# Performance work log

Hardware: AMD Instinct MI355X
Metric: run time of the kernel (lower is better)

## Reference

```python
import jax, jax.numpy as jnp
import numpy as np

N_NODES = 100000
N_EDGES = 3200000
N_GRAPHS = 512
HID = 64
OUT = 10


def setup_inputs() -> dict:
    key = jax.random.key(0)
    ks = jax.random.split(key, 10)
    x = jax.random.normal(ks[0], (N_NODES,), dtype=jnp.float32)
    edge_index = jax.random.randint(ks[1], (2, N_EDGES), 0, N_NODES, dtype=jnp.int64)
    batch = jnp.sort(jax.random.randint(ks[2], (N_NODES,), 0, N_GRAPHS, dtype=jnp.int64))
    # GCNConv weights (glorot) and zero biases, Linear layer params
    W1 = jax.random.normal(ks[3], (1, HID), dtype=jnp.float32) * (1.0 / np.sqrt(1 + HID))
    b1 = jnp.zeros((HID,), dtype=jnp.float32)
    W2 = jax.random.normal(ks[4], (HID, HID), dtype=jnp.float32) * (1.0 / np.sqrt(2 * HID))
    b2 = jnp.zeros((HID,), dtype=jnp.float32)
    Wl = jax.random.normal(ks[5], (2 * HID, OUT), dtype=jnp.float32) * (1.0 / np.sqrt(2 * HID))
    bl = jnp.zeros((OUT,), dtype=jnp.float32)
    return {"x": x, "edge_index": edge_index, "batch": batch,
            "W1": W1, "b1": b1, "W2": W2, "b2": b2, "Wl": Wl, "bl": bl}


def reference(x, edge_index, batch, W1, b1, W2, b2, Wl, bl):
    N = x.shape[0]
    loop = jnp.arange(N, dtype=edge_index.dtype)
    src = jnp.concatenate([edge_index[0], loop])  # add self-loops
    dst = jnp.concatenate([edge_index[1], loop])
    # symmetric GCN normalization: D^{-1/2} A_hat D^{-1/2}
    deg = jax.ops.segment_sum(jnp.ones_like(dst, dtype=jnp.float32), dst, num_segments=N)
    dinv = jax.lax.rsqrt(jnp.maximum(deg, 1.0))
    norm = (dinv[src] * dinv[dst])[:, None]  # [E+N, 1]

    def gcn(h, W, b):
        m = (h @ W)[src] * norm  # transform then gather messages
        return jax.ops.segment_sum(m, dst, num_segments=N) + b

    h0 = x[:, None]  # [N, 1] (dropout is identity at eval)
    x1 = jax.nn.relu(gcn(h0, W1, b1))
    x2 = jax.nn.relu(gcn(x1, W2, b2))
    xj = jnp.concatenate([x1, x2], axis=-1)  # JK 'cat' -> [N, 128]
    # global mean pool per graph
    cnt = jax.ops.segment_sum(jnp.ones((N,), jnp.float32), batch, num_segments=N_GRAPHS)
    pooled = jax.ops.segment_sum(xj, batch, num_segments=N_GRAPHS) / jnp.maximum(cnt, 1.0)[:, None]
    return pooled @ Wl + bl  # [G, 10]
```

## Files before the change

kernel.cpp:

```cpp
#include <hip/hip_runtime.h>
#include <hip/hip_bf16.h>

#define N_NODES 100000
#define N_EDGES 3200000
#define N_GRAPHS 512
#define HID 64
#define OUT_DIM 10

#define NPB 64
#define NB  1563
#define CAP 2432
#define CAP2 (CAP + NPB)


__global__ __launch_bounds__(256) void k_part(const int4* __restrict__ src4,
                                              const int4* __restrict__ dst4,
                                              unsigned* __restrict__ bcur,
                                              unsigned* __restrict__ ebuf) {
    __shared__ unsigned hist[NB];
    int tid = threadIdx.x;
    for (int i = tid; i < NB; i += 256) hist[i] = 0;
    __syncthreads();
    int base4 = (blockIdx.x * 256 + tid) * 2;
    int4 s0 = make_int4(-1, -1, -1, -1), s1 = s0;
    int4 d0 = make_int4(0, 0, 0, 0), d1 = d0;
    if (base4 < N_EDGES / 4)     { s0 = src4[base4];     d0 = dst4[base4]; }
    if (base4 + 1 < N_EDGES / 4) { s1 = src4[base4 + 1]; d1 = dst4[base4 + 1]; }
    int sv[8] = { s0.x, s0.y, s0.z, s0.w, s1.x, s1.y, s1.z, s1.w };
    int dv[8] = { d0.x, d0.y, d0.z, d0.w, d1.x, d1.y, d1.z, d1.w };
    int bk[8]; unsigned rk[8];
    #pragma unroll
    for (int k = 0; k < 8; k++) {
        bk[k] = dv[k] >> 6;
        rk[k] = (sv[k] >= 0) ? atomicAdd(&hist[bk[k]], 1u) : 0u;
    }
    __syncthreads();
    for (int i = tid; i < NB; i += 256) {
        unsigned c = hist[i];
        hist[i] = c ? atomicAdd(&bcur[i], c) : 0u;
    }
    __syncthreads();
    #pragma unroll
    for (int k = 0; k < 8; k++) {
        if (sv[k] >= 0) {
            unsigned dl = (unsigned)(dv[k] & 63);
            ebuf[(size_t)bk[k] * CAP + hist[bk[k]] + rk[k]] = (dl << 17) | (unsigned)sv[k];
        }
    }
}

__global__ __launch_bounds__(256) void k_buck1(unsigned* __restrict__ ebuf,
                                               const unsigned* __restrict__ bcur,
                                               const float* __restrict__ x,
                                               unsigned* __restrict__ deg,
                                               float* __restrict__ dinv,
                                               float* __restrict__ g1) {
    __shared__ unsigned cnt[NPB];
    int b = blockIdx.x, tid = threadIdx.x;
    if (tid < NPB) cnt[tid] = 0;
    __syncthreads();
    int ec = (int)bcur[b];
    unsigned* eb = ebuf + (size_t)b * CAP;
    for (int i = tid; i < ec; i += 256) {
        unsigned w = eb[i];
        unsigned rk = atomicAdd(&cnt[(w >> 17) & 63], 1u);
        eb[i] = w | (rk << 23);
    }
    __syncthreads();
    int n0 = b * NPB;
    int nn = min(NPB, N_NODES - n0);
    if (tid < nn) {
        unsigned c = cnt[tid];
        float dn = 1.0f / sqrtf((float)c + 1.0f);
        deg[n0 + tid] = c;
        dinv[n0 + tid] = dn;
        g1[n0 + tid] = dn * x[n0 + tid];
    }
}

__global__ __launch_bounds__(256) void k_buck2(const unsigned* __restrict__ ebuf,
                                               const unsigned* __restrict__ bcur,
                                               const float* __restrict__ g1,
                                               const float* __restrict__ dinv,
                                               const float* __restrict__ x,
                                               float2* __restrict__ sd) {
    __shared__ float sacc[NPB];
    int b = blockIdx.x, tid = threadIdx.x;
    if (tid < NPB) sacc[tid] = 0.f;
    __syncthreads();
    int ec = (int)bcur[b];
    const unsigned* eb = ebuf + (size_t)b * CAP;
    for (int i = tid; i < ec; i += 256) {
        unsigned w = eb[i];
        atomicAdd(&sacc[(w >> 17) & 63], g1[w & 0x1FFFFu]);
    }
    __syncthreads();
    int n0 = b * NPB;
    int nn = min(NPB, N_NODES - n0);
    if (tid < nn) {
        float dn = dinv[n0 + tid];
        float s = dn * (sacc[tid] + dn * x[n0 + tid]);
        sd[n0 + tid] = make_float2(s, dn);
    }
}

__global__ __launch_bounds__(256) void k_buck3(const unsigned* __restrict__ ebuf,
                                               const unsigned* __restrict__ bcur,
                                               const unsigned* __restrict__ deg,
                                               const float2* __restrict__ sd,
                                               const int* __restrict__ batch,
                                               const float* __restrict__ W1,
                                               const float* __restrict__ b1,
                                               const float* __restrict__ W2,
                                               const float* __restrict__ b2,
                                               float* __restrict__ pooled) {
    __shared__ __align__(16) float2 stage2[CAP2];
    __shared__ float w2ls[HID * HID];
    __shared__ int offs[NPB + 1];
    __shared__ int degs[NPB];
    int b = blockIdx.x, tid = threadIdx.x;
    int lane = tid & 63, wv = tid >> 6;
    int n0 = b * NPB;
    int nn = min(NPB, N_NODES - n0);
    for (int i = tid; i < HID * HID; i += 256) w2ls[i] = W2[i];
    if (wv == 0) {
        int d = (lane < nn) ? (int)deg[n0 + lane] : 0;
        degs[lane] = d;
        int dp = (d + 1) & ~1;
        int sum = dp;
        #pragma unroll
        for (int o = 1; o < 64; o <<= 1) {
            int t = __shfl_up(sum, o, 64);
            if (lane >= o) sum += t;
        }
        offs[lane + 1] = sum;
        offs[lane]     = sum - dp;
        if (lane == 0) offs[0] = 0;
    }
    float w1 = W1[lane], bb1 = b1[lane], bb2 = b2[lane];
    __syncthreads();
    int ec = (int)bcur[b];
    const unsigned* eb = ebuf + (size_t)b * CAP;
    for (int i = tid; i < ec; i += 256) {
        unsigned w = eb[i];
        stage2[offs[(w >> 17) & 63] + (w >> 23)] = sd[w & 0x1FFFFu];
    }
    __syncthreads();
    const float4* stv = (const float4*)stage2;
    int curg = -1;
    float pacc1 = 0.f, pacc2 = 0.f;
    for (int n = wv; n < nn; n += 4) {
        int lo = offs[n];
        int m = degs[n];
        float acca = 0.f, accb = 0.f;
        int half = m >> 1;
        int p0 = lo >> 1;
        for (int k = 0; k < half; k++) {
            float4 e = stv[p0 + k];
            acca = fmaf(e.y, fmaxf(fmaf(e.x, w1, bb1), 0.f), acca);
            accb = fmaf(e.w, fmaxf(fmaf(e.z, w1, bb1), 0.f), accb);
        }
        if (m & 1) {
            float2 e0 = stage2[lo + m - 1];
            acca = fmaf(e0.y, fmaxf(fmaf(e0.x, w1, bb1), 0.f), acca);
        }
        float2 self = sd[n0 + n];
        float t = fmaxf(fmaf(self.x, w1, bb1), 0.f);
        float a = self.y * (acca + accb + self.y * t);
        float acc2a = bb2, acc2b = 0.f;
        #pragma unroll
        for (int j = 0; j < HID; j += 2) {
            float aj0 = __int_as_float(__builtin_amdgcn_readlane(__float_as_int(a), j));
            float aj1 = __int_as_float(__builtin_amdgcn_readlane(__float_as_int(a), j + 1));
            acc2a = fmaf(aj0, w2ls[j * HID + lane], acc2a);
            acc2b = fmaf(aj1, w2ls[(j + 1) * HID + lane], acc2b);
        }
        float x2v = fmaxf(acc2a + acc2b, 0.f);
        int g = batch[n0 + n];
        if (g != curg) {
            if (curg >= 0) {
                atomicAdd(&pooled[curg * 2 * HID + lane], pacc1);
                atomicAdd(&pooled[curg * 2 * HID + HID + lane], pacc2);
            }
            curg = g; pacc1 = 0.f; pacc2 = 0.f;
        }
        pacc1 += t;
        pacc2 += x2v;
    }
    if (curg >= 0) {
        atomicAdd(&pooled[curg * 2 * HID + lane], pacc1);
        atomicAdd(&pooled[curg * 2 * HID + HID + lane], pacc2);
    }
}

__global__ __launch_bounds__(128) void k_head(const float* __restrict__ pooled,
                                              const int* __restrict__ batch,
                                              const float* __restrict__ Wl,
                                              const float* __restrict__ bl,
                                              float* __restrict__ out) {
    int g = blockIdx.x;
    int t = threadIdx.x;
    int lo1 = 0, hi1 = N_NODES;
    while (lo1 < hi1) { int mid = (lo1 + hi1) >> 1; if (batch[mid] < g) lo1 = mid + 1; else hi1 = mid; }
    int lo2 = lo1, hi2 = N_NODES;
    while (lo2 < hi2) { int mid = (lo2 + hi2) >> 1; if (batch[mid] < g + 1) lo2 = mid + 1; else hi2 = mid; }
    float denom = fmaxf((float)(lo2 - lo1), 1.f);
    __shared__ float pl[2 * HID];
    pl[t] = pooled[g * 2 * HID + t] / denom;
    __syncthreads();
    if (t < OUT_DIM) {
        float r = bl[t];
        #pragma unroll 16
        for (int j = 0; j < 2 * HID; j++) r = fmaf(pl[j], Wl[j * OUT_DIM + t], r);
        out[g * OUT_DIM + t] = r;
    }
}

extern "C" void kernel_launch(void* const* d_in, const int* in_sizes, int n_in,
                              void* d_out, int out_size, void* d_ws, size_t ws_size,
                              hipStream_t stream) {
    const float* x      = (const float*)d_in[0];
    const int*   ei     = (const int*)d_in[1];
    const int*   batch  = (const int*)d_in[2];
    const float* W1     = (const float*)d_in[3];
    const float* b1     = (const float*)d_in[4];
    const float* W2     = (const float*)d_in[5];
    const float* b2     = (const float*)d_in[6];
    const float* Wl     = (const float*)d_in[7];
    const float* bl     = (const float*)d_in[8];
    float* out = (float*)d_out;

    const int* src = ei;
    const int* dst = ei + N_EDGES;

    char* p = (char*)d_ws;
    auto alloc = [&](size_t bytes) { void* r = (void*)p; p += (bytes + 255) & ~(size_t)255; return r; };
    unsigned* bcur   = (unsigned*)alloc(NB * 4);
    unsigned* ebuf   = (unsigned*)alloc((size_t)NB * CAP * 4);
    unsigned* deg    = (unsigned*)alloc(N_NODES * 4);
    float*    dinv   = (float*)alloc(N_NODES * 4);
    float*    g1     = (float*)alloc(N_NODES * 4);
    float2*   sd     = (float2*)alloc((size_t)N_NODES * 8);
    float*    pooled = (float*)alloc((size_t)N_GRAPHS * 2 * HID * 4);

    hipMemsetAsync(bcur, 0, NB * 4, stream);
    hipMemsetAsync(pooled, 0, (size_t)N_GRAPHS * 2 * HID * 4, stream);

    const int TB = 256;
    int pbl = (N_EDGES / 8 + TB - 1) / TB;

    k_part <<<pbl, TB, 0, stream>>>((const int4*)src, (const int4*)dst, bcur, ebuf);
    k_buck1<<<NB, TB, 0, stream>>>(ebuf, bcur, x, deg, dinv, g1);
    k_buck2<<<NB, TB, 0, stream>>>(ebuf, bcur, g1, dinv, x, sd);
    k_buck3<<<NB, TB, 0, stream>>>(ebuf, bcur, deg, sd, batch, W1, b1, W2, b2, pooled);
    k_head <<<N_GRAPHS, 128, 0, stream>>>(pooled, batch, Wl, bl, out);
}
```

Before: 266.9 us.

## Replace single-pass edge bucketing with two-level coarse/fine counting sort

Edges are now first scattered into 391 coarse buckets of 256 destination nodes, using larger per-block edge chunks and fewer histogram bins. A second kernel then counting-sorts each coarse bucket by local destination in shared memory and writes a dst-sorted buffer plus per-64-node fine ranges. The later kernels read contiguous fine ranges, which removes the per-edge rank rewrite and gives more coalesced scatter writes in the partition step. The cost is an extra full pass over the edge buffer, a second edge buffer, and a serial single-thread prefix scan over 256 bins per coarse block.

Measured after the change: 251.5 us. -5.8%, faster.

```diff
diff --git a/kernel.cpp b/kernel.cpp
--- a/kernel.cpp
+++ b/kernel.cpp
@@ -7,68 +7,91 @@
 #define HID 64
 #define OUT_DIM 10
 
+#define NPC 256
+#define NCB 391
+#define CAPA 8960
 #define NPB 64
-#define NB  1563
-#define CAP 2432
-#define CAP2 (CAP + NPB)
-
-
-__global__ __launch_bounds__(256) void k_part(const int4* __restrict__ src4,
-                                              const int4* __restrict__ dst4,
-                                              unsigned* __restrict__ bcur,
-                                              unsigned* __restrict__ ebuf) {
-    __shared__ unsigned hist[NB];
+#define NFB 1563
+#define CAPF 2432
+#define CAP2 (CAPF + NPB)
+
+
+__global__ __launch_bounds__(256) void k_partA(const int4* __restrict__ src4,
+                                               const int4* __restrict__ dst4,
+                                               unsigned* __restrict__ bcurA,
+                                               unsigned* __restrict__ ebufA) {
+    __shared__ unsigned hist[NCB];
+    __shared__ unsigned short rk16[4096];
     int tid = threadIdx.x;
-    for (int i = tid; i < NB; i += 256) hist[i] = 0;
-    __syncthreads();
-    int base4 = (blockIdx.x * 256 + tid) * 2;
-    int4 s0 = make_int4(-1, -1, -1, -1), s1 = s0;
-    int4 d0 = make_int4(0, 0, 0, 0), d1 = d0;
-    if (base4 < N_EDGES / 4)     { s0 = src4[base4];     d0 = dst4[base4]; }
-    if (base4 + 1 < N_EDGES / 4) { s1 = src4[base4 + 1]; d1 = dst4[base4 + 1]; }
-    int sv[8] = { s0.x, s0.y, s0.z, s0.w, s1.x, s1.y, s1.z, s1.w };
-    int dv[8] = { d0.x, d0.y, d0.z, d0.w, d1.x, d1.y, d1.z, d1.w };
-    int bk[8]; unsigned rk[8];
+    for (int i = tid; i < NCB; i += 256) hist[i] = 0;
+    __syncthreads();
+    int blk4 = blockIdx.x * 1024;
     #pragma unroll
-    for (int k = 0; k < 8; k++) {
-        bk[k] = dv[k] >> 6;
-        rk[k] = (sv[k] >= 0) ? atomicAdd(&hist[bk[k]], 1u) : 0u;
-    }
-    __syncthreads();
-    for (int i = tid; i < NB; i += 256) {
+    for (int k = 0; k < 4; k++) {
+        int i4 = blk4 + k * 256 + tid;
+        if (i4 < N_EDGES / 4) {
+            int4 d = dst4[i4];
+            int li = (k * 256 + tid) * 4;
+            rk16[li + 0] = (unsigned short)atomicAdd(&hist[d.x >> 8], 1u);
+            rk16[li + 1] = (unsigned short)atomicAdd(&hist[d.y >> 8], 1u);
+            rk16[li + 2] = (unsigned short)atomicAdd(&hist[d.z >> 8], 1u);
+            rk16[li + 3] = (unsigned short)atomicAdd(&hist[d.w >> 8], 1u);
+        }
+    }
+    __syncthreads();
+    for (int i = tid; i < NCB; i += 256) {
         unsigned c = hist[i];
-        hist[i] = c ? atomicAdd(&bcur[i], c) : 0u;
+        hist[i] = c ? atomicAdd(&bcurA[i], c) : 0u;
     }
     __syncthreads();
     #pragma unroll
-    for (int k = 0; k < 8; k++) {
-        if (sv[k] >= 0) {
-            unsigned dl = (unsigned)(dv[k] & 63);
-            ebuf[(size_t)bk[k] * CAP + hist[bk[k]] + rk[k]] = (dl << 17) | (unsigned)sv[k];
-        }
-    }
-}
-
-__global__ __launch_bounds__(256) void k_buck1(unsigned* __restrict__ ebuf,
-                                               const unsigned* __restrict__ bcur,
+    for (int k = 0; k < 4; k++) {
+        int i4 = blk4 + k * 256 + tid;
+        if (i4 < N_EDGES / 4) {
+            int4 s = src4[i4];
+            int4 d = dst4[i4];
+            int li = (k * 256 + tid) * 4;
+            int ss[4] = { s.x, s.y, s.z, s.w };
+            int dd[4] = { d.x, d.y, d.z, d.w };
+            #pragma unroll
+            for (int m = 0; m < 4; m++) {
+                int b = dd[m] >> 8;
+                unsigned dl = (unsigned)(dd[m] & 255);
+                ebufA[(size_t)b * CAPA + hist[b] + rk16[li + m]] = (dl << 17) | (unsigned)ss[m];
+            }
+        }
+    }
+}
+
+__global__ __launch_bounds__(256) void k_partB(const unsigned* __restrict__ ebufA,
+                                               const unsigned* __restrict__ bcurA,
                                                const float* __restrict__ x,
                                                unsigned* __restrict__ deg,
                                                float* __restrict__ dinv,
-                                               float* __restrict__ g1) {
-    __shared__ unsigned cnt[NPB];
-    int b = blockIdx.x, tid = threadIdx.x;
-    if (tid < NPB) cnt[tid] = 0;
-    __syncthreads();
-    int ec = (int)bcur[b];
-    unsigned* eb = ebuf + (size_t)b * CAP;
-    for (int i = tid; i < ec; i += 256) {
-        unsigned w = eb[i];
-        unsigned rk = atomicAdd(&cnt[(w >> 17) & 63], 1u);
-        eb[i] = w | (rk << 23);
-    }
-    __syncthreads();
-    int n0 = b * NPB;
-    int nn = min(NPB, N_NODES - n0);
+                                               float* __restrict__ g1,
+                                               unsigned* __restrict__ ebufB,
+                                               int* __restrict__ fineStart,
+                                               int* __restrict__ fineCnt) {
+    __shared__ unsigned cnt[NPC];
+    __shared__ int offs[NPC + 1];
+    __shared__ unsigned short rk16[CAPA];
+    __shared__ unsigned sorted[CAPA];
+    int cb = blockIdx.x, tid = threadIdx.x;
+    int n0 = cb * NPC;
+    int nn = min(NPC, N_NODES - n0);
+    if (tid < NPC) cnt[tid] = 0;
+    __syncthreads();
+    int ec = (int)bcurA[cb];
+    const unsigned* eb = ebufA + (size_t)cb * CAPA;
+    for (int i = tid; i < ec; i += 256)
+        rk16[i] = (unsigned short)atomicAdd(&cnt[eb[i] >> 17], 1u);
+    __syncthreads();
+    if (tid == 0) {
+        int r = 0;
+        for (int i = 0; i < NPC; i++) { offs[i] = r; r += (int)cnt[i]; }
+        offs[NPC] = r;
+    }
+    __syncthreads();
     if (tid < nn) {
         unsigned c = cnt[tid];
         float dn = 1.0f / sqrtf((float)c + 1.0f);
@@ -76,26 +99,45 @@
         dinv[n0 + tid] = dn;
         g1[n0 + tid] = dn * x[n0 + tid];
     }
-}
-
-__global__ __launch_bounds__(256) void k_buck2(const unsigned* __restrict__ ebuf,
-                                               const unsigned* __restrict__ bcur,
+    if (tid < 4) {
+        int fb = cb * 4 + tid;
+        if (fb < NFB) {
+            int a = tid * 64;
+            int bnd = min(a + 64, nn);
+            int st = (a < nn) ? offs[a] : offs[nn];
+            int en = (a < nn) ? offs[bnd] : offs[nn];
+            fineStart[fb] = (int)((size_t)cb * CAPA) + st;
+            fineCnt[fb] = en - st;
+        }
+    }
+    for (int i = tid; i < ec; i += 256) {
+        unsigned w = eb[i];
+        unsigned dl8 = w >> 17;
+        sorted[offs[dl8] + rk16[i]] = ((dl8 & 63u) << 17) | (w & 0x1FFFFu);
+    }
+    __syncthreads();
+    unsigned* ob = ebufB + (size_t)cb * CAPA;
+    for (int i = tid; i < ec; i += 256) ob[i] = sorted[i];
+}
+
+__global__ __launch_bounds__(256) void k_buck2(const unsigned* __restrict__ ebufB,
+                                               const int* __restrict__ fineStart,
+                                               const int* __restrict__ fineCnt,
                                                const float* __restrict__ g1,
                                                const float* __restrict__ dinv,
                                                const float* __restrict__ x,
                                                float2* __restrict__ sd) {
     __shared__ float sacc[NPB];
-    int b = blockIdx.x, tid = threadIdx.x;
+    int fb = blockIdx.x, tid = threadIdx.x;
     if (tid < NPB) sacc[tid] = 0.f;
     __syncthreads();
-    int ec = (int)bcur[b];
-    const unsigned* eb = ebuf + (size_t)b * CAP;
+    int st = fineStart[fb], ec = fineCnt[fb];
     for (int i = tid; i < ec; i += 256) {
-        unsigned w = eb[i];
-        atomicAdd(&sacc[(w >> 17) & 63], g1[w & 0x1FFFFu]);
-    }
-    __syncthreads();
-    int n0 = b * NPB;
+        unsigned w = ebufB[st + i];
+        atomicAdd(&sacc[(w >> 17) & 63u], g1[w & 0x1FFFFu]);
+    }
+    __syncthreads();
+    int n0 = fb * NPB;
     int nn = min(NPB, N_NODES - n0);
     if (tid < nn) {
         float dn = dinv[n0 + tid];
@@ -104,8 +146,9 @@
     }
 }
 
-__global__ __launch_bounds__(256) void k_buck3(const unsigned* __restrict__ ebuf,
-                                               const unsigned* __restrict__ bcur,
+__global__ __launch_bounds__(256) void k_buck3(const unsigned* __restrict__ ebufB,
+                                               const int* __restrict__ fineStart,
+                                               const int* __restrict__ fineCnt,
                                                const unsigned* __restrict__ deg,
                                                const float2* __restrict__ sd,
                                                const int* __restrict__ batch,
@@ -116,41 +159,44 @@
                                                float* __restrict__ pooled) {
     __shared__ __align__(16) float2 stage2[CAP2];
     __shared__ float w2ls[HID * HID];
-    __shared__ int offs[NPB + 1];
+    __shared__ int poffs[NPB + 1];
+    __shared__ int nstart[NPB];
     __shared__ int degs[NPB];
-    int b = blockIdx.x, tid = threadIdx.x;
+    int fb = blockIdx.x, tid = threadIdx.x;
     int lane = tid & 63, wv = tid >> 6;
-    int n0 = b * NPB;
+    int n0 = fb * NPB;
     int nn = min(NPB, N_NODES - n0);
     for (int i = tid; i < HID * HID; i += 256) w2ls[i] = W2[i];
     if (wv == 0) {
         int d = (lane < nn) ? (int)deg[n0 + lane] : 0;
         degs[lane] = d;
         int dp = (d + 1) & ~1;
-        int sum = dp;
+        int s1 = dp, s2 = d;
         #pragma unroll
         for (int o = 1; o < 64; o <<= 1) {
-            int t = __shfl_up(sum, o, 64);
-            if (lane >= o) sum += t;
-        }
-        offs[lane + 1] = sum;
-        offs[lane]     = sum - dp;
-        if (lane == 0) offs[0] = 0;
+            int t1 = __shfl_up(s1, o, 64);
+            int t2 = __shfl_up(s2, o, 64);
+            if (lane >= o) { s1 += t1; s2 += t2; }
+        }
+        poffs[lane + 1] = s1;
+        poffs[lane]     = s1 - dp;
+        if (lane == 0) poffs[0] = 0;
+        nstart[lane] = s2 - d;
     }
     float w1 = W1[lane], bb1 = b1[lane], bb2 = b2[lane];
     __syncthreads();
-    int ec = (int)bcur[b];
-    const unsigned* eb = ebuf + (size_t)b * CAP;
+    int st = fineStart[fb], ec = fineCnt[fb];
     for (int i = tid; i < ec; i += 256) {
-        unsigned w = eb[i];
-        stage2[offs[(w >> 17) & 63] + (w >> 23)] = sd[w & 0x1FFFFu];
+        unsigned w = ebufB[st + i];
+        int dl = (int)((w >> 17) & 63u);
+        stage2[poffs[dl] + (i - nstart[dl])] = sd[w & 0x1FFFFu];
     }
     __syncthreads();
     const float4* stv = (const float4*)stage2;
     int curg = -1;
     float pacc1 = 0.f, pacc2 = 0.f;
     for (int n = wv; n < nn; n += 4) {
-        int lo = offs[n];
+        int lo = poffs[n];
         int m = degs[n];
         float acca = 0.f, accb = 0.f;
         int half = m >> 1;
@@ -235,23 +281,26 @@
 
     char* p = (char*)d_ws;
     auto alloc = [&](size_t bytes) { void* r = (void*)p; p += (bytes + 255) & ~(size_t)255; return r; };
-    unsigned* bcur   = (unsigned*)alloc(NB * 4);
-    unsigned* ebuf   = (unsigned*)alloc((size_t)NB * CAP * 4);
-    unsigned* deg    = (unsigned*)alloc(N_NODES * 4);
-    float*    dinv   = (float*)alloc(N_NODES * 4);
-    float*    g1     = (float*)alloc(N_NODES * 4);
-    float2*   sd     = (float2*)alloc((size_t)N_NODES * 8);
-    float*    pooled = (float*)alloc((size_t)N_GRAPHS * 2 * HID * 4);
-
-    hipMemsetAsync(bcur, 0, NB * 4, stream);
+    unsigned* bcurA    = (unsigned*)alloc(NCB * 4);
+    unsigned* ebufA    = (unsigned*)alloc((size_t)NCB * CAPA * 4);
+    unsigned* ebufB    = (unsigned*)alloc((size_t)NCB * CAPA * 4);
+    unsigned* deg      = (unsigned*)alloc(N_NODES * 4);
+    float*    dinv     = (float*)alloc(N_NODES * 4);
+    float*    g1       = (float*)alloc(N_NODES * 4);
+    float2*   sd       = (float2*)alloc((size_t)N_NODES * 8);
+    int*      fineStart= (int*)alloc(NFB * 4);
+    int*      fineCnt  = (int*)alloc(NFB * 4);
+    float*    pooled   = (float*)alloc((size_t)N_GRAPHS * 2 * HID * 4);
+
+    hipMemsetAsync(bcurA, 0, NCB * 4, stream);
     hipMemsetAsync(pooled, 0, (size_t)N_GRAPHS * 2 * HID * 4, stream);
 
     const int TB = 256;
-    int pbl = (N_EDGES / 8 + TB - 1) / TB;
-
-    k_part <<<pbl, TB, 0, stream>>>((const int4*)src, (const int4*)dst, bcur, ebuf);
-    k_buck1<<<NB, TB, 0, stream>>>(ebuf, bcur, x, deg, dinv, g1);
-    k_buck2<<<NB, TB, 0, stream>>>(ebuf, bcur, g1, dinv, x, sd);
-    k_buck3<<<NB, TB, 0, stream>>>(ebuf, bcur, deg, sd, batch, W1, b1, W2, b2, pooled);
+    int abl = (N_EDGES / 4 + 1023) / 1024;
+
+    k_partA<<<abl, TB, 0, stream>>>((const int4*)src, (const int4*)dst, bcurA, ebufA);
+    k_partB<<<NCB, TB, 0, stream>>>(ebufA, bcurA, x, deg, dinv, g1, ebufB, fineStart, fineCnt);
+    k_buck2<<<NFB, TB, 0, stream>>>(ebufB, fineStart, fineCnt, g1, dinv, x, sd);
+    k_buck3<<<NFB, TB, 0, stream>>>(ebufB, fineStart, fineCnt, deg, sd, batch, W1, b1, W2, b2, pooled);
     k_head <<<N_GRAPHS, 128, 0, stream>>>(pooled, batch, Wl, bl, out);
 }
```
